# Performance work log

Measured on AMD Instinct MI355X. Metric: run time of the kernel, lower is better.

The kernel has to match this reference:

```python
import jax, jax.numpy as jnp
import numpy as np

BREAKING_TOKENS = jnp.array([13], dtype=jnp.int64)
NUM_HEADS = 16

B, S, E = 2, 2048, 1024


def setup_inputs() -> dict:
    key = jax.random.key(0)
    k1, k2, k3, k4, k5, k6 = jax.random.split(key, 6)
    scale = 1.0 / np.sqrt(E)
    return {
        "input_embeddings": jax.random.normal(k1, (B, S, E), dtype=jnp.float32),
        "token_ids": jax.random.randint(k2, (B, S), 0, 100, dtype=jnp.int64),
        "in_proj_weight": jax.random.normal(k3, (3 * E, E), dtype=jnp.float32) * scale,
        "in_proj_bias": jax.random.normal(k4, (3 * E,), dtype=jnp.float32) * 0.02,
        "out_proj_weight": jax.random.normal(k5, (E, E), dtype=jnp.float32) * scale,
        "out_proj_bias": jax.random.normal(k6, (E,), dtype=jnp.float32) * 0.02,
    }


def _sentence_mask(token_ids):
    # Faithful vectorization of the triple Python loop:
    # mask[b, i, j] is True iff j <= i and no breaking token occurs at positions j..i.
    brk = jnp.isin(token_ids, BREAKING_TOKENS)            # [B, S] bool
    s = jnp.cumsum(brk.astype(jnp.int32), axis=-1)        # inclusive cumsum of breaks
    s_prev = s - brk.astype(jnp.int32)                    # cumsum up to j-1
    seq = token_ids.shape[-1]
    causal = jnp.tril(jnp.ones((seq, seq), dtype=bool))   # j <= i
    # no break in [j, i]  <=>  s[i] == s_prev[j]
    return causal[None, :, :] & (s[:, :, None] == s_prev[:, None, :])  # [B, S, S]


def reference(input_embeddings, token_ids, in_proj_weight, in_proj_bias,
              out_proj_weight, out_proj_bias):
    x = input_embeddings
    b, s, e = x.shape
    h = NUM_HEADS
    d = e // h

    # torch bool attn_mask semantics: True = NOT allowed to attend (-inf).
    mask_true = _sentence_mask(token_ids)                 # [B, S, S]

    qkv = x @ in_proj_weight.T + in_proj_bias             # [B, S, 3E]
    q, k, v = jnp.split(qkv, 3, axis=-1)
    q = q.reshape(b, s, h, d)
    k = k.reshape(b, s, h, d)
    v = v.reshape(b, s, h, d)

    scores = jnp.einsum("bqhd,bkhd->bhqk", q, k) / jnp.sqrt(jnp.asarray(d, x.dtype))
    scores = jnp.where(mask_true[:, None, :, :], -jnp.inf, scores)
    attn = jax.nn.softmax(scores, axis=-1)                # [B, H, S, S]

    out = jnp.einsum("bhqk,bkhd->bqhd", attn, v).reshape(b, s, e)
    return out @ out_proj_weight.T + out_proj_bias
```

## Files before the change

### kernel.cpp

```cpp
#include <hip/hip_runtime.h>
#include <math.h>
#include <stdint.h>

#define BB 2
#define SS 2048
#define EE 1024
#define HH 16
#define DD 64
#define E3 3072
#define NR (BB*SS)

#define C2Q 0.18033688011112042f

typedef __attribute__((ext_vector_type(8))) short short8;
typedef __attribute__((ext_vector_type(4))) float f32x4;

__device__ __forceinline__ ushort f2bf(float f) {
    uint u = __float_as_uint(f);
    uint r = u + 0x7FFFu + ((u >> 16) & 1u);
    return (ushort)(r >> 16);
}
__device__ __forceinline__ short8 pack8(float4 a, float4 b) {
    short8 v;
    v[0] = (short)f2bf(a.x); v[1] = (short)f2bf(a.y); v[2] = (short)f2bf(a.z); v[3] = (short)f2bf(a.w);
    v[4] = (short)f2bf(b.x); v[5] = (short)f2bf(b.y); v[6] = (short)f2bf(b.z); v[7] = (short)f2bf(b.w);
    return v;
}
__device__ __forceinline__ uint cvtpk(float lo, float hi) {
    uint d;
    asm("v_cvt_pk_bf16_f32 %0, %1, %2" : "=v"(d) : "v"(lo), "v"(hi));
    return d;
}

__global__ __launch_bounds__(256) void cvt_bf16(const float* __restrict__ in,
                                                ushort* __restrict__ out, int n8) {
    int i = blockIdx.x * 256 + threadIdx.x;
    if (i < n8) {
        const float4* p = (const float4*)in + (size_t)i * 2;
        float4 a = p[0], b = p[1];
        *((short8*)out + i) = pack8(a, b);
    }
}

__global__ void scan_kernel(const int* __restrict__ tok, int* __restrict__ lbrk) {
    int b = blockIdx.x;
    int t = threadIdx.x;
    __shared__ int pmax[256];
    int loc[8];
    int base = b * SS + t * 8;
    int lm = -1;
#pragma unroll
    for (int i = 0; i < 8; i++) {
        if (tok[base + i] == 13) lm = t * 8 + i;
        loc[i] = lm;
    }
    pmax[t] = lm;
    __syncthreads();
    if (t == 0) {
        int acc = -1;
        for (int i = 0; i < 256; i++) { int tmp = pmax[i]; pmax[i] = acc; acc = max(acc, tmp); }
    }
    __syncthreads();
    int off = pmax[t];
#pragma unroll
    for (int i = 0; i < 8; i++)
        lbrk[base + i] = max(off, loc[i]);
}

template<int OUT_BF16>
__global__ __launch_bounds__(256) void gemm_mfma(const ushort* __restrict__ A,
                                                 const ushort* __restrict__ Bw,
                                                 const float* __restrict__ bias,
                                                 void* __restrict__ Cv,
                                                 int M, int K) {
    __shared__ ushort As[2][128 * 32];
    __shared__ ushort Bs[2][128 * 32];
    const int bm = blockIdx.x * 128;
    const int bn = blockIdx.y * 128;
    const int tid = threadIdx.x;
    const int w = tid >> 6, lane = tid & 63;
    const int l16 = lane & 15, lk = lane >> 4;
    const int wr = w >> 1, wc = w & 1;

    f32x4 acc[4][4];
#pragma unroll
    for (int mi = 0; mi < 4; mi++)
#pragma unroll
        for (int ni = 0; ni < 4; ni++)
            acc[mi][ni] = (f32x4){0.f, 0.f, 0.f, 0.f};

    const int ci  = w * 2;
    const int rA0 = lane >> 2;
    const int gsh = (lane & 3) ^ ((lane >> 2) & 3);

#define GSTAGE(buf, k0)                                                                      \
    {                                                                                        \
        _Pragma("unroll") for (int i2 = 0; i2 < 2; ++i2) {                                   \
            int c = ci + i2;                                                                 \
            int r = c * 16 + rA0;                                                            \
            const ushort* ga = A + (size_t)(bn + r) * K + (k0) + gsh * 8;                    \
            const ushort* gb = Bw + (size_t)(bm + r) * K + (k0) + gsh * 8;                   \
            __builtin_amdgcn_global_load_lds(                                                \
                (const __attribute__((address_space(1))) void*)ga,                           \
                (__attribute__((address_space(3))) void*)((char*)&As[buf][0] + c * 1024),    \
                16, 0, 0);                                                                   \
            __builtin_amdgcn_global_load_lds(                                                \
                (const __attribute__((address_space(1))) void*)gb,                           \
                (__attribute__((address_space(3))) void*)((char*)&Bs[buf][0] + c * 1024),    \
                16, 0, 0);                                                                   \
        }                                                                                    \
    }

    const int pp = (lk ^ (l16 & 3)) * 8;
    const int NT = K / 32;

    GSTAGE(0, 0);
    __syncthreads();

    for (int t = 0; t < NT; ++t) {
        int cur = t & 1;
        if (t + 1 < NT) GSTAGE(cur ^ 1, (t + 1) * 32);
        const ushort* Ab = &As[cur][0];
        const ushort* Bb = &Bs[cur][0];
        short8 af[4], bfr[4];
#pragma unroll
        for (int mi = 0; mi < 4; ++mi) {
            int r = wr * 64 + mi * 16 + l16;
            af[mi] = *(const short8*)(Ab + r * 32 + pp);
        }
#pragma unroll
        for (int ni = 0; ni < 4; ++ni) {
            int r = wc * 64 + ni * 16 + l16;
            bfr[ni] = *(const short8*)(Bb + r * 32 + pp);
        }
#pragma unroll
        for (int mi = 0; mi < 4; ++mi)
#pragma unroll
            for (int ni = 0; ni < 4; ++ni)
                acc[mi][ni] = __builtin_amdgcn_mfma_f32_16x16x32_bf16(af[mi], bfr[ni], acc[mi][ni], 0, 0, 0);
        __syncthreads();
    }
#undef GSTAGE

#pragma unroll
    for (int ni = 0; ni < 4; ++ni) {
        int col = bm + wc * 64 + ni * 16 + l16;
        float bv = bias[col];
#pragma unroll
        for (int mi = 0; mi < 4; ++mi) {
            int row = bn + wr * 64 + mi * 16 + lk * 4;
#pragma unroll
            for (int j = 0; j < 4; ++j) {
                float vv = acc[mi][ni][j] + bv;
                if (OUT_BF16 && col < EE) vv *= C2Q;
                if (OUT_BF16)
                    ((ushort*)Cv)[(size_t)(row + j) * M + col] = f2bf(vv);
                else
                    ((float*)Cv)[(size_t)(row + j) * M + col] = vv;
            }
        }
    }
}

__global__ __launch_bounds__(256) void vtrans(const ushort* __restrict__ qkv,
                                              ushort* __restrict__ vT) {
    __shared__ __align__(16) ushort ts[64][72];
    const int bid = blockIdx.x;
    const int jt = bid & 31;
    const int h  = (bid >> 5) & 15;
    const int b  = bid >> 9;
    const int tid = threadIdx.x;
    {
        int j = tid >> 2, cg = tid & 3;
        const ushort* src = qkv + (size_t)(b * SS + jt * 64 + j) * E3 + 2 * EE + h * DD + cg * 16;
        uint4 u0 = ((const uint4*)src)[0];
        uint4 u1 = ((const uint4*)src)[1];
        *(uint4*)&ts[j][cg * 16]     = u0;
        *(uint4*)&ts[j][cg * 16 + 8] = u1;
    }
    __syncthreads();
    {
        int d = tid & 63, jg = tid >> 6;
        uint v[8];
#pragma unroll
        for (int p = 0; p < 8; p++)
            v[p] = (uint)ts[jg * 16 + 2 * p][d] | ((uint)ts[jg * 16 + 2 * p + 1][d] << 16);
        ushort* dst = vT + ((size_t)((b * HH + h) * DD + d)) * SS + jt * 64 + jg * 16;
        *(uint4*)dst       = make_uint4(v[0], v[1], v[2], v[3]);
        *(uint4*)(dst + 8) = make_uint4(v[4], v[5], v[6], v[7]);
    }
}

__global__ __launch_bounds__(256, 4) void attn_mfma(const ushort* __restrict__ qkv,
                                                    const ushort* __restrict__ vT,
                                                    const int* __restrict__ lbrk,
                                                    ushort* __restrict__ ao) {
    __shared__ ushort ks[2][64 * 64];
    __shared__ ushort vt[2][64 * 64];
    __shared__ ushort ps[4 * 16 * 64];

    int bid = (blockIdx.x & 7) * 128 + (blockIdx.x >> 3);
    const int qt = bid & 31;
    const int h  = (bid >> 5) & 15;
    const int b  = bid >> 9;
    const int q0 = qt * 64;
    const int tid = threadIdx.x;
    const int w    = tid >> 6;
    const int lane = tid & 63;
    const int l16  = lane & 15;
    const int lk   = lane >> 4;
    const int swz8 = (l16 & 7) << 3;

    const ushort* qkv_b = qkv + (size_t)(b * SS) * E3;
    const ushort* vT_bh = vT + ((size_t)(b * HH + h)) * DD * SS;

    const int qrow = q0 + w * 16 + l16;
    const int lbq  = lbrk[b * SS + qrow];
    const int lb1  = lbq + 1;
    const uint wid = (uint)(qrow - lbq);

    short8 qf[2];
#pragma unroll
    for (int kk = 0; kk < 2; kk++)
        qf[kk] = *(const short8*)(qkv_b + (size_t)qrow * E3 + h * DD + kk * 32 + lk * 8);

    const int srow = lane >> 3;
    const int slot = lane & 7;
    const ushort* gK[2];
    const ushort* gV[2];
#pragma unroll
    for (int i = 0; i < 2; i++) {
        int r = w * 16 + i * 8 + srow;
        int sl = (slot ^ (r & 7)) << 3;
        gK[i] = qkv_b + (size_t)r * E3 + EE + h * DD + sl;
        gV[i] = vT_bh + (size_t)r * SS + sl;
    }

#define STAGE(buf, kt)                                                                        \
    {                                                                                         \
        _Pragma("unroll") for (int i = 0; i < 2; ++i) {                                       \
            __builtin_amdgcn_global_load_lds(                                                 \
                (const __attribute__((address_space(1))) void*)(gK[i] + (size_t)(kt) * 64 * E3), \
                (__attribute__((address_space(3))) void*)((char*)&ks[buf][0] + w * 2048 + i * 1024), \
                16, 0, 0);                                                                    \
            __builtin_amdgcn_global_load_lds(                                                 \
                (const __attribute__((address_space(1))) void*)(gV[i] + (size_t)(kt) * 64),   \
                (__attribute__((address_space(3))) void*)((char*)&vt[buf][0] + w * 2048 + i * 1024), \
                16, 0, 0);                                                                    \
        }                                                                                     \
    }

    short8 ones8;
#pragma unroll
    for (int i = 0; i < 8; i++) ones8[i] = (short)0x3F80;

    f32x4 o[4];
    f32x4 o_l = (f32x4){0.f, 0.f, 0.f, 0.f};
#pragma unroll
    for (int n = 0; n < 4; n++) o[n] = (f32x4){0.f, 0.f, 0.f, 0.f};

    ushort* pw = &ps[w * 1024];

    STAGE(0, 0);

    for (int t = 0; t < 32; ++t) {
        const int cur = t & 1;
        if (t < 31) {
            STAGE(cur ^ 1, t + 1);
            asm volatile("s_waitcnt vmcnt(4)" ::: "memory");
        } else {
            asm volatile("s_waitcnt vmcnt(0)" ::: "memory");
        }
        __builtin_amdgcn_s_barrier();

        const ushort* kb = &ks[cur][0];
        const ushort* vb = &vt[cur][0];

        f32x4 s[4];
#pragma unroll
        for (int n = 0; n < 4; n++) s[n] = (f32x4){0.f, 0.f, 0.f, 0.f};
#pragma unroll
        for (int n = 0; n < 4; n++) {
#pragma unroll
            for (int kk = 0; kk < 2; kk++) {
                short8 kf = *(const short8*)(kb + (n * 16 + l16) * 64 + (((4 * kk + lk) ^ (l16 & 7)) << 3));
                s[n] = __builtin_amdgcn_mfma_f32_16x16x32_bf16(kf, qf[kk], s[n], 0, 0, 0);
            }
        }

        const int jb0 = t * 64 + lk * 4 - lb1;
#pragma unroll
        for (int n = 0; n < 4; n++) {
            const int jbn = jb0 + n * 16;
            float p0, p1, p2, p3;
            {
                uint j0 = (uint)(jbn + 0), j1 = (uint)(jbn + 1);
                uint j2 = (uint)(jbn + 2), j3 = (uint)(jbn + 3);
                p0 = exp2f(j0 < wid ? -1e30f : s[n][0]);
                p1 = exp2f(j1 < wid ? -1e30f : s[n][1]);
                p2 = exp2f(j2 < wid ? -1e30f : s[n][2]);
                p3 = exp2f(j3 < wid ? -1e30f : s[n][3]);
            }
            uint d0 = cvtpk(p0, p1);
            uint d1 = cvtpk(p2, p3);
            int col = (n * 16 + lk * 4) ^ swz8;
            *(uint*)(pw + l16 * 64 + col)     = d0;
            *(uint*)(pw + l16 * 64 + col + 2) = d1;
        }

        short8 pf[2];
#pragma unroll
        for (int kk = 0; kk < 2; kk++)
            pf[kk] = *(const short8*)(pw + l16 * 64 + (((4 * kk + lk) ^ (l16 & 7)) << 3));

#pragma unroll
        for (int kk = 0; kk < 2; kk++)
            o_l = __builtin_amdgcn_mfma_f32_16x16x32_bf16(pf[kk], ones8, o_l, 0, 0, 0);

#pragma unroll
        for (int n = 0; n < 4; n++) {
#pragma unroll
            for (int kk = 0; kk < 2; kk++) {
                short8 vf = *(const short8*)(vb + (n * 16 + l16) * 64 + (((4 * kk + lk) ^ (l16 & 7)) << 3));
                o[n] = __builtin_amdgcn_mfma_f32_16x16x32_bf16(pf[kk], vf, o[n], 0, 0, 0);
            }
        }

        asm volatile("s_waitcnt lgkmcnt(0)" ::: "memory");
        __builtin_amdgcn_s_barrier();
    }
#undef STAGE

    float inv[4];
#pragma unroll
    for (int r = 0; r < 4; r++) inv[r] = 1.f / o_l[r];
#pragma unroll
    for (int n = 0; n < 4; n++) {
#pragma unroll
        for (int r = 0; r < 4; r++) {
            int qo = q0 + w * 16 + lk * 4 + r;
            ao[(size_t)(b * SS + qo) * EE + h * DD + n * 16 + l16] = f2bf(o[n][r] * inv[r]);
        }
    }
}

extern "C" void kernel_launch(void* const* d_in, const int* in_sizes, int n_in,
                              void* d_out, int out_size, void* d_ws, size_t ws_size,
                              hipStream_t stream) {
    const float* x    = (const float*)d_in[0];
    const int*   tok  = (const int*)d_in[1];
    const float* win  = (const float*)d_in[2];
    const float* bin  = (const float*)d_in[3];
    const float* wout = (const float*)d_in[4];
    const float* bout = (const float*)d_in[5];
    float* out = (float*)d_out;

    ushort* xb    = (ushort*)d_ws;
    ushort* winb  = xb + (size_t)NR * EE;
    ushort* woutb = winb + (size_t)E3 * EE;
    ushort* qkvb  = woutb + (size_t)EE * EE;
    ushort* aob   = qkvb + (size_t)NR * E3;
    ushort* vTb   = aob + (size_t)NR * EE;
    int* lbrk  = (int*)(vTb + (size_t)BB * HH * DD * SS);

    int nx8 = NR * EE / 8, nwin8 = E3 * EE / 8, nwout8 = EE * EE / 8;
    cvt_bf16<<<(nx8 + 255) / 256, 256, 0, stream>>>(x, xb, nx8);
    cvt_bf16<<<(nwin8 + 255) / 256, 256, 0, stream>>>(win, winb, nwin8);
    cvt_bf16<<<(nwout8 + 255) / 256, 256, 0, stream>>>(wout, woutb, nwout8);

    scan_kernel<<<BB, 256, 0, stream>>>(tok, lbrk);

    gemm_mfma<1><<<dim3(E3 / 128, NR / 128), 256, 0, stream>>>(xb, winb, bin, (void*)qkvb, E3, EE);

    vtrans<<<BB * HH * (SS / 64), 256, 0, stream>>>(qkvb, vTb);

    attn_mfma<<<BB * HH * (SS / 64), 256, 0, stream>>>(qkvb, vTb, lbrk, aob);

    gemm_mfma<0><<<dim3(EE / 128, NR / 128), 256, 0, stream>>>(aob, woutb, bout, (void*)out, EE, EE);
}
```

Baseline: 153.0 us.

## Enlarge attention query tile, keep P in registers, and permute V transpose layout

Each attention block now covers 256 queries (64 per wave) rather than 64, so every staged K/V tile is reused across four query groups and global K/V traffic drops. S is computed transposed so the softmax probabilities can be fed straight from registers as the MFMA B operand, removing the LDS round trip for P. vtrans writes V with a permuted key order to match that register layout. Staging becomes a two-tile prefetch issued after the barrier, and the mask check is skipped for tiles where no query can be masked. The cost is more accumulator registers per wave (occupancy hint dropped) and only 256 blocks in the grid.

```diff
diff --git a/kernel.cpp b/kernel.cpp
--- a/kernel.cpp
+++ b/kernel.cpp
@@ -14,6 +14,7 @@
 
 typedef __attribute__((ext_vector_type(8))) short short8;
 typedef __attribute__((ext_vector_type(4))) float f32x4;
+typedef __attribute__((ext_vector_type(4))) uint uint4v;
 
 __device__ __forceinline__ ushort f2bf(float f) {
     uint u = __float_as_uint(f);
@@ -180,49 +181,62 @@
     }
     __syncthreads();
     {
-        int d = tid & 63, jg = tid >> 6;
-        uint v[8];
-#pragma unroll
-        for (int p = 0; p < 8; p++)
-            v[p] = (uint)ts[jg * 16 + 2 * p][d] | ((uint)ts[jg * 16 + 2 * p + 1][d] << 16);
-        ushort* dst = vT + ((size_t)((b * HH + h) * DD + d)) * SS + jt * 64 + jg * 16;
-        *(uint4*)dst       = make_uint4(v[0], v[1], v[2], v[3]);
-        *(uint4*)(dst + 8) = make_uint4(v[4], v[5], v[6], v[7]);
-    }
-}
-
-__global__ __launch_bounds__(256, 4) void attn_mfma(const ushort* __restrict__ qkv,
-                                                    const ushort* __restrict__ vT,
-                                                    const int* __restrict__ lbrk,
-                                                    ushort* __restrict__ ao) {
+        int d = tid & 63, cq = tid >> 6;
+        ushort vals[16];
+#pragma unroll
+        for (int cc = 0; cc < 16; ++cc) {
+            int c = cq * 16 + cc;
+            int t32 = c >> 5, c5 = c & 31;
+            int a = c5 >> 3, hi = (c5 >> 2) & 1, i = c5 & 3;
+            int j = t32 * 32 + hi * 16 + a * 4 + i;
+            vals[cc] = ts[j][d];
+        }
+        ushort* dst = vT + ((size_t)((b * HH + h) * DD + d)) * SS + jt * 64 + cq * 16;
+        uint4 o0, o1;
+        o0.x = (uint)vals[0] | ((uint)vals[1] << 16);  o0.y = (uint)vals[2] | ((uint)vals[3] << 16);
+        o0.z = (uint)vals[4] | ((uint)vals[5] << 16);  o0.w = (uint)vals[6] | ((uint)vals[7] << 16);
+        o1.x = (uint)vals[8] | ((uint)vals[9] << 16);  o1.y = (uint)vals[10] | ((uint)vals[11] << 16);
+        o1.z = (uint)vals[12] | ((uint)vals[13] << 16); o1.w = (uint)vals[14] | ((uint)vals[15] << 16);
+        *(uint4*)dst       = o0;
+        *(uint4*)(dst + 8) = o1;
+    }
+}
+
+__global__ __launch_bounds__(256) void attn_mfma(const ushort* __restrict__ qkv,
+                                                 const ushort* __restrict__ vT,
+                                                 const int* __restrict__ lbrk,
+                                                 ushort* __restrict__ ao) {
     __shared__ ushort ks[2][64 * 64];
     __shared__ ushort vt[2][64 * 64];
-    __shared__ ushort ps[4 * 16 * 64];
-
-    int bid = (blockIdx.x & 7) * 128 + (blockIdx.x >> 3);
-    const int qt = bid & 31;
-    const int h  = (bid >> 5) & 15;
-    const int b  = bid >> 9;
-    const int q0 = qt * 64;
+
+    int bid = (blockIdx.x & 7) * 32 + (blockIdx.x >> 3);
+    const int qb = bid & 7;
+    const int h  = (bid >> 3) & 15;
+    const int b  = bid >> 7;
+    const int q0b = qb * 256;
     const int tid = threadIdx.x;
-    const int w    = tid >> 6;
-    const int lane = tid & 63;
-    const int l16  = lane & 15;
-    const int lk   = lane >> 4;
-    const int swz8 = (l16 & 7) << 3;
+    const int w = tid >> 6, lane = tid & 63;
+    const int l16 = lane & 15, lk = lane >> 4;
+    const int q0w = q0b + w * 64;
 
     const ushort* qkv_b = qkv + (size_t)(b * SS) * E3;
     const ushort* vT_bh = vT + ((size_t)(b * HH + h)) * DD * SS;
 
-    const int qrow = q0 + w * 16 + l16;
-    const int lbq  = lbrk[b * SS + qrow];
-    const int lb1  = lbq + 1;
-    const uint wid = (uint)(qrow - lbq);
-
-    short8 qf[2];
-#pragma unroll
-    for (int kk = 0; kk < 2; kk++)
-        qf[kk] = *(const short8*)(qkv_b + (size_t)qrow * E3 + h * DD + kk * 32 + lk * 8);
+    short8 qf[4][2];
+#pragma unroll
+    for (int qg = 0; qg < 4; qg++)
+#pragma unroll
+        for (int kk = 0; kk < 2; kk++)
+            qf[qg][kk] = *(const short8*)(qkv_b + (size_t)(q0w + qg * 16 + l16) * E3 + h * DD + kk * 32 + lk * 8);
+
+    int lb1[4]; uint wid[4];
+#pragma unroll
+    for (int qg = 0; qg < 4; qg++) {
+        int q = q0w + qg * 16 + l16;
+        int lb = lbrk[b * SS + q];
+        lb1[qg] = lb + 1;
+        wid[qg] = (uint)(q - lb);
+    }
 
     const int srow = lane >> 3;
     const int slot = lane & 7;
@@ -236,110 +250,126 @@
         gV[i] = vT_bh + (size_t)r * SS + sl;
     }
 
-#define STAGE(buf, kt)                                                                        \
-    {                                                                                         \
-        _Pragma("unroll") for (int i = 0; i < 2; ++i) {                                       \
-            __builtin_amdgcn_global_load_lds(                                                 \
-                (const __attribute__((address_space(1))) void*)(gK[i] + (size_t)(kt) * 64 * E3), \
+#define STAGE(buf, kt)                                                                            \
+    {                                                                                             \
+        _Pragma("unroll") for (int i = 0; i < 2; ++i) {                                           \
+            __builtin_amdgcn_global_load_lds(                                                     \
+                (const __attribute__((address_space(1))) void*)(gK[i] + (size_t)(kt) * 64 * E3),  \
                 (__attribute__((address_space(3))) void*)((char*)&ks[buf][0] + w * 2048 + i * 1024), \
-                16, 0, 0);                                                                    \
-            __builtin_amdgcn_global_load_lds(                                                 \
-                (const __attribute__((address_space(1))) void*)(gV[i] + (size_t)(kt) * 64),   \
+                16, 0, 0);                                                                        \
+            __builtin_amdgcn_global_load_lds(                                                     \
+                (const __attribute__((address_space(1))) void*)(gV[i] + (size_t)(kt) * 64),       \
                 (__attribute__((address_space(3))) void*)((char*)&vt[buf][0] + w * 2048 + i * 1024), \
-                16, 0, 0);                                                                    \
-        }                                                                                     \
-    }
+                16, 0, 0);                                                                        \
+        }                                                                                         \
+    }
+
+    const int xr = l16 & 7;
+    int perm[2];
+#pragma unroll
+    for (int u = 0; u < 2; u++) perm[u] = ((u * 4 + lk) ^ xr) << 3;
 
     short8 ones8;
 #pragma unroll
     for (int i = 0; i < 8; i++) ones8[i] = (short)0x3F80;
 
-    f32x4 o[4];
-    f32x4 o_l = (f32x4){0.f, 0.f, 0.f, 0.f};
-#pragma unroll
-    for (int n = 0; n < 4; n++) o[n] = (f32x4){0.f, 0.f, 0.f, 0.f};
-
-    ushort* pw = &ps[w * 1024];
+    f32x4 o[4][4];
+    f32x4 l_acc[4];
+#pragma unroll
+    for (int dg = 0; dg < 4; dg++)
+#pragma unroll
+        for (int qg = 0; qg < 4; qg++)
+            o[dg][qg] = (f32x4){0.f, 0.f, 0.f, 0.f};
+#pragma unroll
+    for (int qg = 0; qg < 4; qg++) l_acc[qg] = (f32x4){0.f, 0.f, 0.f, 0.f};
+
+    const int tmask = qb * 4 + 3;
 
     STAGE(0, 0);
+    STAGE(1, 1);
 
     for (int t = 0; t < 32; ++t) {
-        const int cur = t & 1;
-        if (t < 31) {
-            STAGE(cur ^ 1, t + 1);
-            asm volatile("s_waitcnt vmcnt(4)" ::: "memory");
-        } else {
-            asm volatile("s_waitcnt vmcnt(0)" ::: "memory");
-        }
+        if (t < 31) asm volatile("s_waitcnt vmcnt(4)" ::: "memory");
+        else        asm volatile("s_waitcnt vmcnt(0)" ::: "memory");
         __builtin_amdgcn_s_barrier();
 
-        const ushort* kb = &ks[cur][0];
-        const ushort* vb = &vt[cur][0];
-
-        f32x4 s[4];
-#pragma unroll
-        for (int n = 0; n < 4; n++) s[n] = (f32x4){0.f, 0.f, 0.f, 0.f};
-#pragma unroll
-        for (int n = 0; n < 4; n++) {
-#pragma unroll
-            for (int kk = 0; kk < 2; kk++) {
-                short8 kf = *(const short8*)(kb + (n * 16 + l16) * 64 + (((4 * kk + lk) ^ (l16 & 7)) << 3));
-                s[n] = __builtin_amdgcn_mfma_f32_16x16x32_bf16(kf, qf[kk], s[n], 0, 0, 0);
+        const ushort* kb = &ks[t & 1][0];
+        const ushort* vb = &vt[t & 1][0];
+        const bool domask = (t <= tmask);
+
+#pragma unroll
+        for (int t32 = 0; t32 < 2; ++t32) {
+            uint pu[4][4];
+#pragma unroll
+            for (int hi = 0; hi < 2; ++hi) {
+                const int jg = t32 * 2 + hi;
+                short8 kf0 = *(const short8*)(kb + (jg * 16 + l16) * 64 + perm[0]);
+                short8 kf1 = *(const short8*)(kb + (jg * 16 + l16) * 64 + perm[1]);
+                f32x4 s[4];
+#pragma unroll
+                for (int qg = 0; qg < 4; qg++) {
+                    s[qg] = (f32x4){0.f, 0.f, 0.f, 0.f};
+                    s[qg] = __builtin_amdgcn_mfma_f32_16x16x32_bf16(kf0, qf[qg][0], s[qg], 0, 0, 0);
+                    s[qg] = __builtin_amdgcn_mfma_f32_16x16x32_bf16(kf1, qf[qg][1], s[qg], 0, 0, 0);
+                }
+                const int jbase = t * 64 + t32 * 32 + hi * 16 + lk * 4;
+#pragma unroll
+                for (int qg = 0; qg < 4; qg++) {
+                    float p0, p1, p2, p3;
+                    if (domask) {
+                        int jb = jbase - lb1[qg];
+                        p0 = exp2f((uint)(jb + 0) < wid[qg] ? -1e30f : s[qg][0]);
+                        p1 = exp2f((uint)(jb + 1) < wid[qg] ? -1e30f : s[qg][1]);
+                        p2 = exp2f((uint)(jb + 2) < wid[qg] ? -1e30f : s[qg][2]);
+                        p3 = exp2f((uint)(jb + 3) < wid[qg] ? -1e30f : s[qg][3]);
+                    } else {
+                        p0 = exp2f(s[qg][0]);
+                        p1 = exp2f(s[qg][1]);
+                        p2 = exp2f(s[qg][2]);
+                        p3 = exp2f(s[qg][3]);
+                    }
+                    pu[qg][hi * 2]     = cvtpk(p0, p1);
+                    pu[qg][hi * 2 + 1] = cvtpk(p2, p3);
+                }
             }
-        }
-
-        const int jb0 = t * 64 + lk * 4 - lb1;
-#pragma unroll
-        for (int n = 0; n < 4; n++) {
-            const int jbn = jb0 + n * 16;
-            float p0, p1, p2, p3;
-            {
-                uint j0 = (uint)(jbn + 0), j1 = (uint)(jbn + 1);
-                uint j2 = (uint)(jbn + 2), j3 = (uint)(jbn + 3);
-                p0 = exp2f(j0 < wid ? -1e30f : s[n][0]);
-                p1 = exp2f(j1 < wid ? -1e30f : s[n][1]);
-                p2 = exp2f(j2 < wid ? -1e30f : s[n][2]);
-                p3 = exp2f(j3 < wid ? -1e30f : s[n][3]);
+            short8 pfB[4];
+#pragma unroll
+            for (int qg = 0; qg < 4; qg++) {
+                uint4v u;
+                u[0] = pu[qg][0]; u[1] = pu[qg][1]; u[2] = pu[qg][2]; u[3] = pu[qg][3];
+                pfB[qg] = __builtin_bit_cast(short8, u);
             }
-            uint d0 = cvtpk(p0, p1);
-            uint d1 = cvtpk(p2, p3);
-            int col = (n * 16 + lk * 4) ^ swz8;
-            *(uint*)(pw + l16 * 64 + col)     = d0;
-            *(uint*)(pw + l16 * 64 + col + 2) = d1;
-        }
-
-        short8 pf[2];
-#pragma unroll
-        for (int kk = 0; kk < 2; kk++)
-            pf[kk] = *(const short8*)(pw + l16 * 64 + (((4 * kk + lk) ^ (l16 & 7)) << 3));
-
-#pragma unroll
-        for (int kk = 0; kk < 2; kk++)
-            o_l = __builtin_amdgcn_mfma_f32_16x16x32_bf16(pf[kk], ones8, o_l, 0, 0, 0);
-
-#pragma unroll
-        for (int n = 0; n < 4; n++) {
-#pragma unroll
-            for (int kk = 0; kk < 2; kk++) {
-                short8 vf = *(const short8*)(vb + (n * 16 + l16) * 64 + (((4 * kk + lk) ^ (l16 & 7)) << 3));
-                o[n] = __builtin_amdgcn_mfma_f32_16x16x32_bf16(pf[kk], vf, o[n], 0, 0, 0);
+#pragma unroll
+            for (int qg = 0; qg < 4; qg++)
+                l_acc[qg] = __builtin_amdgcn_mfma_f32_16x16x32_bf16(ones8, pfB[qg], l_acc[qg], 0, 0, 0);
+#pragma unroll
+            for (int dg = 0; dg < 4; dg++) {
+                short8 vf = *(const short8*)(vb + (dg * 16 + l16) * 64 + perm[t32]);
+#pragma unroll
+                for (int qg = 0; qg < 4; qg++)
+                    o[dg][qg] = __builtin_amdgcn_mfma_f32_16x16x32_bf16(vf, pfB[qg], o[dg][qg], 0, 0, 0);
             }
         }
 
         asm volatile("s_waitcnt lgkmcnt(0)" ::: "memory");
         __builtin_amdgcn_s_barrier();
+        if (t + 2 < 32) STAGE(t & 1, t + 2);
     }
 #undef STAGE
 
     float inv[4];
 #pragma unroll
-    for (int r = 0; r < 4; r++) inv[r] = 1.f / o_l[r];
-#pragma unroll
-    for (int n = 0; n < 4; n++) {
-#pragma unroll
-        for (int r = 0; r < 4; r++) {
-            int qo = q0 + w * 16 + lk * 4 + r;
-            ao[(size_t)(b * SS + qo) * EE + h * DD + n * 16 + l16] = f2bf(o[n][r] * inv[r]);
+    for (int qg = 0; qg < 4; qg++) inv[qg] = 1.f / l_acc[qg][0];
+#pragma unroll
+    for (int qg = 0; qg < 4; qg++) {
+        int qo = q0w + qg * 16 + l16;
+        ushort* dst = ao + (size_t)(b * SS + qo) * EE + h * DD + lk * 4;
+#pragma unroll
+        for (int dg = 0; dg < 4; dg++) {
+            uint u0 = cvtpk(o[dg][qg][0] * inv[qg], o[dg][qg][1] * inv[qg]);
+            uint u1 = cvtpk(o[dg][qg][2] * inv[qg], o[dg][qg][3] * inv[qg]);
+            uint2 pk; pk.x = u0; pk.y = u1;
+            *(uint2*)(dst + dg * 16) = pk;
         }
     }
 }
@@ -374,7 +404,7 @@
 
     vtrans<<<BB * HH * (SS / 64), 256, 0, stream>>>(qkvb, vTb);
 
-    attn_mfma<<<BB * HH * (SS / 64), 256, 0, stream>>>(qkvb, vTb, lbrk, aob);
+    attn_mfma<<<BB * HH * (SS / 256), 256, 0, stream>>>(qkvb, vTb, lbrk, aob);
 
     gemm_mfma<0><<<dim3(EE / 128, NR / 128), 256, 0, stream>>>(aob, woutb, bout, (void*)out, EE, EE);
 }
```

Result: slower. 197.3 us (+28.9%).
